# Performance work log

Hardware: AMD Instinct MI355X
Metric: run time of the kernel (lower is better)

## Reference

```python
import jax, jax.numpy as jnp
import numpy as np

B, L, D = 4, 4096, 1024


def setup_inputs() -> dict:
    key = jax.random.key(0)
    ks = jax.random.split(key, 10)
    x = jax.random.normal(ks[0], (B, L, D), dtype=jnp.float32)
    time_decay = jax.random.normal(ks[1], (D,), dtype=jnp.float32) * 0.1 - 5.0
    time_first = jax.random.normal(ks[2], (D,), dtype=jnp.float32) * 0.01
    time_mix_k = jnp.ones((D,), jnp.float32) * 0.5
    time_mix_v = jnp.ones((D,), jnp.float32) * 0.5
    time_mix_r = jnp.ones((D,), jnp.float32) * 0.5
    s = 1.0 / np.sqrt(D)
    Wk = jax.random.normal(ks[3], (D, D), dtype=jnp.float32) * s
    Wv = jax.random.normal(ks[4], (D, D), dtype=jnp.float32) * s
    Wr = jax.random.normal(ks[5], (D, D), dtype=jnp.float32) * s
    Wo = jax.random.normal(ks[6], (D, D), dtype=jnp.float32) * s
    return {"x": x, "time_decay": time_decay, "time_first": time_first,
            "time_mix_k": time_mix_k, "time_mix_v": time_mix_v, "time_mix_r": time_mix_r,
            "Wk": Wk, "Wv": Wv, "Wr": Wr, "Wo": Wo}


def _wkv_scan(k, v, w, u):
    # k, v: [B, L, D]; w, u: [D]. Sequential linear recurrence over L.
    decay = jnp.exp(w)  # per-channel decay factor e^{w}, w = -exp(time_decay) < 0
    Bb, Ll, Dd = k.shape

    def step(carry, kv_t):
        a, b = carry  # [B, D] numerator / denominator states
        k_t, v_t = kv_t
        ek_u = jnp.exp(u + k_t)
        wkv = (a + ek_u * v_t) / jnp.maximum(b + ek_u, 1e-6)
        ek = jnp.exp(k_t)
        return (decay * a + ek * v_t, decay * b + ek), wkv

    init = (jnp.zeros((Bb, Dd), k.dtype), jnp.zeros((Bb, Dd), k.dtype))
    _, out = jax.lax.scan(step, init, (jnp.swapaxes(k, 0, 1), jnp.swapaxes(v, 0, 1)))
    return jnp.swapaxes(out, 0, 1)  # [B, L, D]


def reference(x, time_decay, time_first, time_mix_k, time_mix_v, time_mix_r, Wk, Wv, Wr, Wo):
    Ll = x.shape[1]
    # token shift: x_prev[t] = x[t-1], zeros at t=0
    x_prev = jnp.pad(x, ((0, 0), (1, 0), (0, 0)))[:, :Ll]
    xk = x * time_mix_k + x_prev * (1.0 - time_mix_k)
    xv = x * time_mix_v + x_prev * (1.0 - time_mix_v)
    xr = x * time_mix_r + x_prev * (1.0 - time_mix_r)
    k = jnp.einsum('bld,ed->ble', xk, Wk)
    v = jnp.einsum('bld,ed->ble', xv, Wv)
    r = jax.nn.sigmoid(jnp.einsum('bld,ed->ble', xr, Wr))
    w = -jnp.exp(time_decay)
    wkv = _wkv_scan(k, v, w, time_first)
    return jnp.einsum('bld,ed->ble', r * wkv, Wo)
```

## Files before the change

kernel.cpp:

```cpp
#include <hip/hip_runtime.h>
#include <cstdint>
#include <cstddef>

typedef __bf16 bf16;
typedef __bf16 bf16x8 __attribute__((ext_vector_type(8)));
typedef float floatx4 __attribute__((ext_vector_type(4)));
typedef float floatx8 __attribute__((ext_vector_type(8)));
typedef unsigned int u32;

constexpr int Bb = 4, Ll = 4096, Dd = 1024;
constexpr int M  = Bb * Ll;
constexpr int NC = 64, CT = 64;

typedef const __attribute__((address_space(1))) u32 glb_u32;
typedef __attribute__((address_space(3))) u32 lds_u32;
__device__ __forceinline__ void gld16(const bf16* g, bf16* l) {
  __builtin_amdgcn_global_load_lds((glb_u32*)g, (lds_u32*)l, 16, 0, 0);
}

__global__ __launch_bounds__(256) void convw(
    const float* __restrict__ W, bf16* __restrict__ Wb)
{
  size_t base = ((size_t)blockIdx.x * 256 + threadIdx.x) * 8;
  floatx8 w = *(const floatx8*)(W + base);
  bf16x8 o;
  #pragma unroll
  for (int j = 0; j < 8; ++j) o[j] = (bf16)w[j];
  *(bf16x8*)(Wb + base) = o;
}

__global__ __launch_bounds__(256) void prep2(
    const float* __restrict__ x, const float* __restrict__ ma, const float* __restrict__ mb,
    bf16* __restrict__ oa, bf16* __restrict__ ob)
{
  size_t base = ((size_t)blockIdx.x * 256 + threadIdx.x) * 8;
  int d = (int)(base & (size_t)(Dd - 1));
  int l = (int)((base / Dd) & (size_t)(Ll - 1));
  floatx8 xc = *(const floatx8*)(x + base);
  floatx8 xp = l ? *(const floatx8*)(x + base - Dd) : (floatx8)(0.0f);
  floatx8 a = *(const floatx8*)(ma + d);
  floatx8 b = *(const floatx8*)(mb + d);
  bf16x8 ra, rb;
  #pragma unroll
  for (int j = 0; j < 8; ++j) {
    ra[j] = (bf16)(xc[j] * a[j] + xp[j] * (1.0f - a[j]));
    rb[j] = (bf16)(xc[j] * b[j] + xp[j] * (1.0f - b[j]));
  }
  *(bf16x8*)(oa + base) = ra;
  *(bf16x8*)(ob + base) = rb;
}

__global__ __launch_bounds__(256) void prep1(
    const float* __restrict__ x, const float* __restrict__ ma, bf16* __restrict__ oa)
{
  size_t base = ((size_t)blockIdx.x * 256 + threadIdx.x) * 8;
  int d = (int)(base & (size_t)(Dd - 1));
  int l = (int)((base / Dd) & (size_t)(Ll - 1));
  floatx8 xc = *(const floatx8*)(x + base);
  floatx8 xp = l ? *(const floatx8*)(x + base - Dd) : (floatx8)(0.0f);
  floatx8 a = *(const floatx8*)(ma + d);
  bf16x8 ra;
  #pragma unroll
  for (int j = 0; j < 8; ++j)
    ra[j] = (bf16)(xc[j] * a[j] + xp[j] * (1.0f - a[j]));
  *(bf16x8*)(oa + base) = ra;
}

template <int ACT>
__global__ __launch_bounds__(256) void gemm_bb(
    const bf16* __restrict__ A, const bf16* __restrict__ W, void* __restrict__ Cout)
{
  __shared__ __align__(16) bf16 As[128 * 32];
  __shared__ __align__(16) bf16 Bs[128 * 32];
  const int tid  = threadIdx.x;
  const int lane = tid & 63;
  const int w    = tid >> 6;
  const int wm   = (w >> 1) * 64, wn = (w & 1) * 64;
  const int fr   = lane & 15;
  const int cu   = lane >> 4;
  const int soff = ((cu ^ ((fr >> 1) & 3)) << 3);

  const int flat = (int)(blockIdx.y * 8 + blockIdx.x);
  const int nid  = (flat & 7) * 128 + (flat >> 3);
  const int m0   = (nid >> 3) * 128, n0 = (nid & 7) * 128;

  const int u0 = tid, u1 = tid + 256;
  const int r0 = u0 >> 2, c0 = (((u0 & 3) ^ ((r0 >> 1) & 3)) << 3);
  const int r1 = u1 >> 2, c1 = (((u1 & 3) ^ ((r1 >> 1) & 3)) << 3);

  floatx4 acc[4][4];
  #pragma unroll
  for (int i = 0; i < 4; ++i)
    #pragma unroll
    for (int j = 0; j < 4; ++j)
      acc[i][j] = (floatx4)(0.0f);

  for (int k0 = 0; k0 < Dd; k0 += 32) {
    gld16(A + (size_t)(m0 + r0) * Dd + k0 + c0, As + (size_t)u0 * 8);
    gld16(A + (size_t)(m0 + r1) * Dd + k0 + c1, As + (size_t)u1 * 8);
    gld16(W + (size_t)(n0 + r0) * Dd + k0 + c0, Bs + (size_t)u0 * 8);
    gld16(W + (size_t)(n0 + r1) * Dd + k0 + c1, Bs + (size_t)u1 * 8);
    __syncthreads();

    bf16x8 af[4], bfv[4];
    #pragma unroll
    for (int i = 0; i < 4; ++i) af[i]  = *(const bf16x8*)(As + (wm + i * 16 + fr) * 32 + soff);
    #pragma unroll
    for (int j = 0; j < 4; ++j) bfv[j] = *(const bf16x8*)(Bs + (wn + j * 16 + fr) * 32 + soff);
    #pragma unroll
    for (int i = 0; i < 4; ++i)
      #pragma unroll
      for (int j = 0; j < 4; ++j)
        acc[i][j] = __builtin_amdgcn_mfma_f32_16x16x32_bf16(af[i], bfv[j], acc[i][j], 0, 0, 0);
    __syncthreads();
  }

  #pragma unroll
  for (int i = 0; i < 4; ++i) {
    int rbase = m0 + wm + i * 16 + (lane >> 4) * 4;
    #pragma unroll
    for (int j = 0; j < 4; ++j) {
      int col = n0 + wn + j * 16 + (lane & 15);
      #pragma unroll
      for (int r = 0; r < 4; ++r) {
        float v = acc[i][j][r];
        size_t off = (size_t)(rbase + r) * Dd + col;
        if (ACT == 0)      ((float*)Cout)[off] = v;
        else if (ACT == 1) ((bf16*)Cout)[off]  = (bf16)(1.0f / (1.0f + __expf(-v)));
        else               ((bf16*)Cout)[off]  = (bf16)v;
      }
    }
  }
}

__global__ __launch_bounds__(256) void scan_partial(
    const bf16* __restrict__ k, const bf16* __restrict__ v,
    const float* __restrict__ td, float* __restrict__ Pa, float* __restrict__ Pb)
{
  int d = blockIdx.x * 256 + threadIdx.x;
  int b = blockIdx.y, c = blockIdx.z;
  float decay = __expf(-__expf(td[d]));
  size_t base = ((size_t)(b * Ll + c * CT)) * Dd + d;
  float pa = 0.0f, pb = 0.0f;
  #pragma unroll 4
  for (int t = 0; t < CT; ++t) {
    size_t idx = base + (size_t)t * Dd;
    float ek = __expf((float)k[idx]);
    pa = decay * pa + ek * (float)v[idx];
    pb = decay * pb + ek;
  }
  size_t o = ((size_t)(b * NC + c)) * Dd + d;
  Pa[o] = pa; Pb[o] = pb;
}

__global__ __launch_bounds__(256) void scan_combine(
    const float* __restrict__ td, const float* __restrict__ Pa, const float* __restrict__ Pb,
    float* __restrict__ A0, float* __restrict__ B0)
{
  int d = blockIdx.x * 256 + threadIdx.x;
  int b = blockIdx.y;
  float dT = __expf(-__expf(td[d]) * (float)CT);
  float a = 0.0f, bb = 0.0f;
  for (int c = 0; c < NC; ++c) {
    size_t o = ((size_t)(b * NC + c)) * Dd + d;
    A0[o] = a; B0[o] = bb;
    a  = dT * a  + Pa[o];
    bb = dT * bb + Pb[o];
  }
}

__global__ __launch_bounds__(256) void scan_final(
    const bf16* __restrict__ k, bf16* __restrict__ vy, const bf16* __restrict__ r,
    const float* __restrict__ td, const float* __restrict__ tf,
    const float* __restrict__ A0, const float* __restrict__ B0)
{
  int d = blockIdx.x * 256 + threadIdx.x;
  int b = blockIdx.y, c = blockIdx.z;
  float decay = __expf(-__expf(td[d]));
  float u     = tf[d];
  size_t o = ((size_t)(b * NC + c)) * Dd + d;
  float a = A0[o], bb = B0[o];
  size_t base = ((size_t)(b * Ll + c * CT)) * Dd + d;
  for (int t = 0; t < CT; ++t) {
    size_t idx = base + (size_t)t * Dd;
    float kk = (float)k[idx];
    float vv = (float)vy[idx];
    float eku = __expf(u + kk);
    float wkv = (a + eku * vv) / fmaxf(bb + eku, 1e-6f);
    vy[idx] = (bf16)((float)r[idx] * wkv);
    float ek = __expf(kk);
    a  = decay * a  + ek * vv;
    bb = decay * bb + ek;
  }
}

extern "C" void kernel_launch(void* const* d_in, const int* in_sizes, int n_in,
                              void* d_out, int out_size, void* d_ws, size_t ws_size,
                              hipStream_t stream)
{
  const float* x  = (const float*)d_in[0];
  const float* td = (const float*)d_in[1];
  const float* tf = (const float*)d_in[2];
  const float* mk = (const float*)d_in[3];
  const float* mv = (const float*)d_in[4];
  const float* mr = (const float*)d_in[5];
  const float* Wk = (const float*)d_in[6];
  const float* Wv = (const float*)d_in[7];
  const float* Wr = (const float*)d_in[8];
  const float* Wo = (const float*)d_in[9];
  float* out = (float*)d_out;

  char* ws = (char*)d_ws;
  const size_t S2 = (size_t)M * Dd * sizeof(bf16);
  const size_t SP = (size_t)Bb * NC * Dd;
  bf16* buf1 = (bf16*)(ws);
  bf16* buf2 = (bf16*)(ws + S2);
  bf16* buf3 = (bf16*)(ws + 2 * S2);
  float* Pa = (float*)(ws + 3 * S2);
  float* Pb = Pa + SP;
  float* A0 = Pb + SP;
  float* B0 = A0 + SP;

  char* ob  = (char*)d_out;
  bf16* rr  = (bf16*)d_out;
  bf16* Wkb = (bf16*)(ob + ((size_t)32 << 20));
  bf16* Wvb = (bf16*)(ob + ((size_t)34 << 20));
  bf16* Wrb = (bf16*)(ob + ((size_t)36 << 20));
  bf16* Wob = (bf16*)Pa;

  dim3 gp((unsigned)((size_t)M * Dd / (256 * 8)));
  dim3 gw((unsigned)((size_t)Dd * Dd / (256 * 8)));
  dim3 gg(Dd / 128, M / 128);

  convw<<<gw, 256, 0, stream>>>(Wk, Wkb);
  convw<<<gw, 256, 0, stream>>>(Wv, Wvb);
  convw<<<gw, 256, 0, stream>>>(Wr, Wrb);

  prep2<<<gp, 256, 0, stream>>>(x, mk, mv, buf1, buf2);
  gemm_bb<2><<<gg, 256, 0, stream>>>(buf1, Wkb, buf3);
  gemm_bb<2><<<gg, 256, 0, stream>>>(buf2, Wvb, buf1);
  prep1<<<gp, 256, 0, stream>>>(x, mr, buf2);
  gemm_bb<1><<<gg, 256, 0, stream>>>(buf2, Wrb, rr);

  scan_partial<<<dim3(Dd / 256, Bb, NC), 256, 0, stream>>>(buf3, buf1, td, Pa, Pb);
  scan_combine<<<dim3(Dd / 256, Bb), 256, 0, stream>>>(td, Pa, Pb, A0, B0);
  convw<<<gw, 256, 0, stream>>>(Wo, Wob);
  scan_final  <<<dim3(Dd / 256, Bb, NC), 256, 0, stream>>>(buf3, buf1, rr, td, tf, A0, B0);

  gemm_bb<0><<<gg, 256, 0, stream>>>(buf1, Wob, out);
}
```

Baseline: 403.8 us.

## Replace GEMM with 256x256-tile double-buffered 8-wave pipelined kernel

Replaces the 128x128, BK=32, single-buffered bf16 GEMM with a 256x256-tile, BK=64 kernel using 512 threads. It double-buffers LDS (128KB) and splits each k-step into four quarter phases, so global-to-LDS loads of the next tile interleave with MFMA work on the current one. It also uses an XOR swizzle and s_setprio around the MFMA bursts. Separately, the three weight-conversion launches are merged into one kernel. The risks are low occupancy from the large LDS footprint and correctness of the manual vmcnt waits.

```diff
diff --git a/kernel.cpp b/kernel.cpp
--- a/kernel.cpp
+++ b/kernel.cpp
@@ -17,6 +17,10 @@
 __device__ __forceinline__ void gld16(const bf16* g, bf16* l) {
   __builtin_amdgcn_global_load_lds((glb_u32*)g, (lds_u32*)l, 16, 0, 0);
 }
+__device__ __forceinline__ void bar() {
+  __builtin_amdgcn_s_barrier();
+  asm volatile("" ::: "memory");
+}
 
 __global__ __launch_bounds__(256) void convw(
     const float* __restrict__ W, bf16* __restrict__ Wb)
@@ -27,6 +31,20 @@
   #pragma unroll
   for (int j = 0; j < 8; ++j) o[j] = (bf16)w[j];
   *(bf16x8*)(Wb + base) = o;
+}
+
+__global__ __launch_bounds__(256) void convw3(
+    const float* __restrict__ Wa, const float* __restrict__ Wbp, const float* __restrict__ Wc,
+    bf16* __restrict__ oa, bf16* __restrict__ ob, bf16* __restrict__ oc)
+{
+  const float* s = blockIdx.y == 0 ? Wa : (blockIdx.y == 1 ? Wbp : Wc);
+  bf16*        d = blockIdx.y == 0 ? oa : (blockIdx.y == 1 ? ob  : oc);
+  size_t base = ((size_t)blockIdx.x * 256 + threadIdx.x) * 8;
+  floatx8 w = *(const floatx8*)(s + base);
+  bf16x8 o;
+  #pragma unroll
+  for (int j = 0; j < 8; ++j) o[j] = (bf16)w[j];
+  *(bf16x8*)(d + base) = o;
 }
 
 __global__ __launch_bounds__(256) void prep2(
@@ -67,63 +85,158 @@
 }
 
 template <int ACT>
-__global__ __launch_bounds__(256) void gemm_bb(
+__global__ __launch_bounds__(512, 2) void gemm8(
     const bf16* __restrict__ A, const bf16* __restrict__ W, void* __restrict__ Cout)
 {
-  __shared__ __align__(16) bf16 As[128 * 32];
-  __shared__ __align__(16) bf16 Bs[128 * 32];
+  __shared__ __align__(16) bf16 sm[65536];
   const int tid  = threadIdx.x;
   const int lane = tid & 63;
   const int w    = tid >> 6;
-  const int wm   = (w >> 1) * 64, wn = (w & 1) * 64;
+  const int wm   = (w >> 2) * 128;
+  const int wn   = (w & 3) * 64;
   const int fr   = lane & 15;
   const int cu   = lane >> 4;
-  const int soff = ((cu ^ ((fr >> 1) & 3)) << 3);
-
-  const int flat = (int)(blockIdx.y * 8 + blockIdx.x);
-  const int nid  = (flat & 7) * 128 + (flat >> 3);
-  const int m0   = (nid >> 3) * 128, n0 = (nid & 7) * 128;
-
-  const int u0 = tid, u1 = tid + 256;
-  const int r0 = u0 >> 2, c0 = (((u0 & 3) ^ ((r0 >> 1) & 3)) << 3);
-  const int r1 = u1 >> 2, c1 = (((u1 & 3) ^ ((r1 >> 1) & 3)) << 3);
-
-  floatx4 acc[4][4];
-  #pragma unroll
-  for (int i = 0; i < 4; ++i)
+  const int key  = fr & 7;
+  const int sw0  = ((cu)     ^ key) * 8;
+  const int sw1  = ((4 | cu) ^ key) * 8;
+  const int aro  = wm + fr;
+  const int bro  = wn + fr;
+
+  const int flat = (int)(blockIdx.y * 4 + blockIdx.x);
+  const int nid  = (flat & 7) * 32 + (flat >> 3);
+  const int m0   = (nid >> 2) * 256, n0 = (nid & 3) * 256;
+
+  const int w0_ = tid, w1_ = tid + 512;
+  const int lr0 = w0_ >> 3, sc0 = ((w0_ & 7) ^ (lr0 & 7)) * 8;
+  const int lr1 = w1_ >> 3, sc1 = ((w1_ & 7) ^ (lr1 & 7)) * 8;
+  const size_t rA0 = (size_t)(m0 + lr0) * Dd + sc0;
+  const size_t rA1 = (size_t)(m0 + lr1) * Dd + sc1;
+  const size_t rB0 = (size_t)(n0 + lr0) * Dd + sc0;
+  const size_t rB1 = (size_t)(n0 + lr1) * Dd + sc1;
+  const size_t HSTEP = (size_t)128 * Dd;
+
+  floatx4 acc[8][4];
+  #pragma unroll
+  for (int i = 0; i < 8; ++i)
     #pragma unroll
     for (int j = 0; j < 4; ++j)
       acc[i][j] = (floatx4)(0.0f);
 
-  for (int k0 = 0; k0 < Dd; k0 += 32) {
-    gld16(A + (size_t)(m0 + r0) * Dd + k0 + c0, As + (size_t)u0 * 8);
-    gld16(A + (size_t)(m0 + r1) * Dd + k0 + c1, As + (size_t)u1 * 8);
-    gld16(W + (size_t)(n0 + r0) * Dd + k0 + c0, Bs + (size_t)u0 * 8);
-    gld16(W + (size_t)(n0 + r1) * Dd + k0 + c1, Bs + (size_t)u1 * 8);
-    __syncthreads();
-
-    bf16x8 af[4], bfv[4];
-    #pragma unroll
-    for (int i = 0; i < 4; ++i) af[i]  = *(const bf16x8*)(As + (wm + i * 16 + fr) * 32 + soff);
-    #pragma unroll
-    for (int j = 0; j < 4; ++j) bfv[j] = *(const bf16x8*)(Bs + (wn + j * 16 + fr) * 32 + soff);
-    #pragma unroll
-    for (int i = 0; i < 4; ++i)
-      #pragma unroll
-      for (int j = 0; j < 4; ++j)
-        acc[i][j] = __builtin_amdgcn_mfma_f32_16x16x32_bf16(af[i], bfv[j], acc[i][j], 0, 0, 0);
-    __syncthreads();
-  }
-
-  #pragma unroll
-  for (int i = 0; i < 4; ++i) {
-    int rbase = m0 + wm + i * 16 + (lane >> 4) * 4;
+  {
+    bf16* A0 = sm;
+    bf16* B0 = sm + 16384;
+    gld16(A + rA0,         A0 + (size_t)w0_ * 8);
+    gld16(A + rA1,         A0 + (size_t)w1_ * 8);
+    gld16(W + rB0,         B0 + (size_t)w0_ * 8);
+    gld16(W + rB1,         B0 + (size_t)w1_ * 8);
+    gld16(W + rB0 + HSTEP, B0 + 8192 + (size_t)w0_ * 8);
+    gld16(W + rB1 + HSTEP, B0 + 8192 + (size_t)w1_ * 8);
+    gld16(A + rA0 + HSTEP, A0 + 8192 + (size_t)w0_ * 8);
+    gld16(A + rA1 + HSTEP, A0 + 8192 + (size_t)w1_ * 8);
+    asm volatile("s_waitcnt vmcnt(4)" ::: "memory");
+    bar();
+  }
+
+  bf16x8 a[8], bl[4], bh[4];
+  #pragma unroll 2
+  for (int t = 0; t < 16; ++t) {
+    const int p = t & 1;
+    bf16* Ap = sm + p * 32768;
+    bf16* Bp = Ap + 16384;
+    bf16* Aq = sm + (p ^ 1) * 32768;
+    bf16* Bq = Aq + 16384;
+    const size_t kn = (size_t)((t < 15 ? t + 1 : 15) * 64);
+
+    #pragma unroll
+    for (int i = 0; i < 4; ++i) {
+      a[i * 2 + 0] = *(const bf16x8*)(Ap + (aro + i * 16) * 64 + sw0);
+      a[i * 2 + 1] = *(const bf16x8*)(Ap + (aro + i * 16) * 64 + sw1);
+    }
+    #pragma unroll
+    for (int j = 0; j < 2; ++j) {
+      bl[j * 2 + 0] = *(const bf16x8*)(Bp + (bro + j * 16) * 64 + sw0);
+      bl[j * 2 + 1] = *(const bf16x8*)(Bp + (bro + j * 16) * 64 + sw1);
+    }
+    gld16(A + rA0 + kn, Aq + (size_t)w0_ * 8);
+    gld16(A + rA1 + kn, Aq + (size_t)w1_ * 8);
+    asm volatile("s_waitcnt vmcnt(4)" ::: "memory");
+    bar();
+    __builtin_amdgcn_s_setprio(1);
+    #pragma unroll
+    for (int ks = 0; ks < 2; ++ks)
+      #pragma unroll
+      for (int i = 0; i < 4; ++i)
+        #pragma unroll
+        for (int j = 0; j < 2; ++j)
+          acc[i][j] = __builtin_amdgcn_mfma_f32_16x16x32_bf16(a[i * 2 + ks], bl[j * 2 + ks], acc[i][j], 0, 0, 0);
+    __builtin_amdgcn_s_setprio(0);
+    bar();
+
+    #pragma unroll
+    for (int j = 0; j < 2; ++j) {
+      bh[j * 2 + 0] = *(const bf16x8*)(Bp + (bro + (j + 2) * 16) * 64 + sw0);
+      bh[j * 2 + 1] = *(const bf16x8*)(Bp + (bro + (j + 2) * 16) * 64 + sw1);
+    }
+    gld16(W + rB0 + kn, Bq + (size_t)w0_ * 8);
+    gld16(W + rB1 + kn, Bq + (size_t)w1_ * 8);
+    asm volatile("s_waitcnt vmcnt(4)" ::: "memory");
+    bar();
+    __builtin_amdgcn_s_setprio(1);
+    #pragma unroll
+    for (int ks = 0; ks < 2; ++ks)
+      #pragma unroll
+      for (int i = 0; i < 4; ++i)
+        #pragma unroll
+        for (int j = 0; j < 2; ++j)
+          acc[i][j + 2] = __builtin_amdgcn_mfma_f32_16x16x32_bf16(a[i * 2 + ks], bh[j * 2 + ks], acc[i][j + 2], 0, 0, 0);
+    __builtin_amdgcn_s_setprio(0);
+    bar();
+
+    #pragma unroll
+    for (int i = 0; i < 4; ++i) {
+      a[i * 2 + 0] = *(const bf16x8*)(Ap + (aro + (i + 4) * 16) * 64 + sw0);
+      a[i * 2 + 1] = *(const bf16x8*)(Ap + (aro + (i + 4) * 16) * 64 + sw1);
+    }
+    gld16(W + rB0 + kn + HSTEP, Bq + 8192 + (size_t)w0_ * 8);
+    gld16(W + rB1 + kn + HSTEP, Bq + 8192 + (size_t)w1_ * 8);
+    bar();
+    __builtin_amdgcn_s_setprio(1);
+    #pragma unroll
+    for (int ks = 0; ks < 2; ++ks)
+      #pragma unroll
+      for (int i = 0; i < 4; ++i)
+        #pragma unroll
+        for (int j = 0; j < 2; ++j)
+          acc[i + 4][j + 2] = __builtin_amdgcn_mfma_f32_16x16x32_bf16(a[i * 2 + ks], bh[j * 2 + ks], acc[i + 4][j + 2], 0, 0, 0);
+    __builtin_amdgcn_s_setprio(0);
+    bar();
+
+    gld16(A + rA0 + kn + HSTEP, Aq + 8192 + (size_t)w0_ * 8);
+    gld16(A + rA1 + kn + HSTEP, Aq + 8192 + (size_t)w1_ * 8);
+    asm volatile("s_waitcnt vmcnt(4)" ::: "memory");
+    bar();
+    __builtin_amdgcn_s_setprio(1);
+    #pragma unroll
+    for (int ks = 0; ks < 2; ++ks)
+      #pragma unroll
+      for (int i = 0; i < 4; ++i)
+        #pragma unroll
+        for (int j = 0; j < 2; ++j)
+          acc[i + 4][j] = __builtin_amdgcn_mfma_f32_16x16x32_bf16(a[i * 2 + ks], bl[j * 2 + ks], acc[i + 4][j], 0, 0, 0);
+    __builtin_amdgcn_s_setprio(0);
+    bar();
+  }
+  asm volatile("s_waitcnt vmcnt(0)" ::: "memory");
+
+  #pragma unroll
+  for (int mi = 0; mi < 8; ++mi) {
+    int rbase = m0 + wm + mi * 16 + (lane >> 4) * 4;
     #pragma unroll
     for (int j = 0; j < 4; ++j) {
       int col = n0 + wn + j * 16 + (lane & 15);
       #pragma unroll
       for (int r = 0; r < 4; ++r) {
-        float v = acc[i][j][r];
+        float v = acc[mi][j][r];
         size_t off = (size_t)(rbase + r) * Dd + col;
         if (ACT == 0)      ((float*)Cout)[off] = v;
         else if (ACT == 1) ((bf16*)Cout)[off]  = (bf16)(1.0f / (1.0f + __expf(-v)));
@@ -230,22 +343,20 @@
 
   dim3 gp((unsigned)((size_t)M * Dd / (256 * 8)));
   dim3 gw((unsigned)((size_t)Dd * Dd / (256 * 8)));
-  dim3 gg(Dd / 128, M / 128);
-
-  convw<<<gw, 256, 0, stream>>>(Wk, Wkb);
-  convw<<<gw, 256, 0, stream>>>(Wv, Wvb);
-  convw<<<gw, 256, 0, stream>>>(Wr, Wrb);
+  dim3 gg(Dd / 256, M / 256);
+
+  convw3<<<dim3(gw.x, 3), 256, 0, stream>>>(Wk, Wv, Wr, Wkb, Wvb, Wrb);
 
   prep2<<<gp, 256, 0, stream>>>(x, mk, mv, buf1, buf2);
-  gemm_bb<2><<<gg, 256, 0, stream>>>(buf1, Wkb, buf3);
-  gemm_bb<2><<<gg, 256, 0, stream>>>(buf2, Wvb, buf1);
+  gemm8<2><<<gg, 512, 0, stream>>>(buf1, Wkb, buf3);
+  gemm8<2><<<gg, 512, 0, stream>>>(buf2, Wvb, buf1);
   prep1<<<gp, 256, 0, stream>>>(x, mr, buf2);
-  gemm_bb<1><<<gg, 256, 0, stream>>>(buf2, Wrb, rr);
+  gemm8<1><<<gg, 512, 0, stream>>>(buf2, Wrb, rr);
 
   scan_partial<<<dim3(Dd / 256, Bb, NC), 256, 0, stream>>>(buf3, buf1, td, Pa, Pb);
   scan_combine<<<dim3(Dd / 256, Bb), 256, 0, stream>>>(td, Pa, Pb, A0, B0);
   convw<<<gw, 256, 0, stream>>>(Wo, Wob);
   scan_final  <<<dim3(Dd / 256, Bb, NC), 256, 0, stream>>>(buf3, buf1, rr, td, tf, A0, B0);
 
-  gemm_bb<0><<<gg, 256, 0, stream>>>(buf1, Wob, out);
-}
+  gemm8<0><<<gg, 512, 0, stream>>>(buf1, Wob, out);
+}
```

Result: faster. 350.0 us (-13.3%).

## Replace GEMM with 256x256 triple-buffered pipelined kernel and fuse prep kernels

Applied to the files above, without the earlier changes.

The GEMM is rewritten to use 256x256 tiles with 512 threads and a three-slot LDS ring. Global-to-LDS loads are issued two steps ahead and interleaved with MFMA work through sched_group_barrier and setprio, with explicit vmcnt waits. This is meant to hide load latency and reuse each tile more. The three weight conversions are merged into one launch, and the three token-shift preps into one kernel, reordering GEMMs so buffers are freed correctly. The larger tile gives only 256 blocks per GEMM and uses more LDS and registers, which may limit occupancy.

```diff
diff --git a/kernel.cpp b/kernel.cpp
--- a/kernel.cpp
+++ b/kernel.cpp
@@ -17,6 +17,10 @@
 __device__ __forceinline__ void gld16(const bf16* g, bf16* l) {
   __builtin_amdgcn_global_load_lds((glb_u32*)g, (lds_u32*)l, 16, 0, 0);
 }
+__device__ __forceinline__ void bar() {
+  __builtin_amdgcn_s_barrier();
+  asm volatile("" ::: "memory");
+}
 
 __global__ __launch_bounds__(256) void convw(
     const float* __restrict__ W, bf16* __restrict__ Wb)
@@ -29,9 +33,24 @@
   *(bf16x8*)(Wb + base) = o;
 }
 
-__global__ __launch_bounds__(256) void prep2(
+__global__ __launch_bounds__(256) void convw3(
+    const float* __restrict__ Wa, const float* __restrict__ Wbp, const float* __restrict__ Wc,
+    bf16* __restrict__ oa, bf16* __restrict__ ob, bf16* __restrict__ oc)
+{
+  const float* s = blockIdx.y == 0 ? Wa : (blockIdx.y == 1 ? Wbp : Wc);
+  bf16*        d = blockIdx.y == 0 ? oa : (blockIdx.y == 1 ? ob  : oc);
+  size_t base = ((size_t)blockIdx.x * 256 + threadIdx.x) * 8;
+  floatx8 w = *(const floatx8*)(s + base);
+  bf16x8 o;
+  #pragma unroll
+  for (int j = 0; j < 8; ++j) o[j] = (bf16)w[j];
+  *(bf16x8*)(d + base) = o;
+}
+
+__global__ __launch_bounds__(256) void prep3(
     const float* __restrict__ x, const float* __restrict__ ma, const float* __restrict__ mb,
-    bf16* __restrict__ oa, bf16* __restrict__ ob)
+    const float* __restrict__ mc,
+    bf16* __restrict__ oa, bf16* __restrict__ ob, bf16* __restrict__ oc)
 {
   size_t base = ((size_t)blockIdx.x * 256 + threadIdx.x) * 8;
   int d = (int)(base & (size_t)(Dd - 1));
@@ -40,90 +59,137 @@
   floatx8 xp = l ? *(const floatx8*)(x + base - Dd) : (floatx8)(0.0f);
   floatx8 a = *(const floatx8*)(ma + d);
   floatx8 b = *(const floatx8*)(mb + d);
-  bf16x8 ra, rb;
+  floatx8 c = *(const floatx8*)(mc + d);
+  bf16x8 ra, rb, rc;
   #pragma unroll
   for (int j = 0; j < 8; ++j) {
     ra[j] = (bf16)(xc[j] * a[j] + xp[j] * (1.0f - a[j]));
     rb[j] = (bf16)(xc[j] * b[j] + xp[j] * (1.0f - b[j]));
+    rc[j] = (bf16)(xc[j] * c[j] + xp[j] * (1.0f - c[j]));
   }
   *(bf16x8*)(oa + base) = ra;
   *(bf16x8*)(ob + base) = rb;
-}
-
-__global__ __launch_bounds__(256) void prep1(
-    const float* __restrict__ x, const float* __restrict__ ma, bf16* __restrict__ oa)
-{
-  size_t base = ((size_t)blockIdx.x * 256 + threadIdx.x) * 8;
-  int d = (int)(base & (size_t)(Dd - 1));
-  int l = (int)((base / Dd) & (size_t)(Ll - 1));
-  floatx8 xc = *(const floatx8*)(x + base);
-  floatx8 xp = l ? *(const floatx8*)(x + base - Dd) : (floatx8)(0.0f);
-  floatx8 a = *(const floatx8*)(ma + d);
-  bf16x8 ra;
-  #pragma unroll
-  for (int j = 0; j < 8; ++j)
-    ra[j] = (bf16)(xc[j] * a[j] + xp[j] * (1.0f - a[j]));
-  *(bf16x8*)(oa + base) = ra;
+  *(bf16x8*)(oc + base) = rc;
 }
 
 template <int ACT>
-__global__ __launch_bounds__(256) void gemm_bb(
+__global__ __launch_bounds__(512, 2) void gemm8(
     const bf16* __restrict__ A, const bf16* __restrict__ W, void* __restrict__ Cout)
 {
-  __shared__ __align__(16) bf16 As[128 * 32];
-  __shared__ __align__(16) bf16 Bs[128 * 32];
+  __shared__ __align__(16) bf16 sm[49152];
   const int tid  = threadIdx.x;
   const int lane = tid & 63;
   const int w    = tid >> 6;
-  const int wm   = (w >> 1) * 64, wn = (w & 1) * 64;
+  const int wm   = (w >> 2) * 128;
+  const int wn   = (w & 3) * 64;
   const int fr   = lane & 15;
   const int cu   = lane >> 4;
   const int soff = ((cu ^ ((fr >> 1) & 3)) << 3);
-
-  const int flat = (int)(blockIdx.y * 8 + blockIdx.x);
-  const int nid  = (flat & 7) * 128 + (flat >> 3);
-  const int m0   = (nid >> 3) * 128, n0 = (nid & 7) * 128;
-
-  const int u0 = tid, u1 = tid + 256;
+  const int aro  = wm + fr;
+  const int bro  = wn + fr;
+
+  const int flat = (int)(blockIdx.y * 4 + blockIdx.x);
+  const int nid  = (flat & 7) * 32 + (flat >> 3);
+  const int m0   = (nid >> 2) * 256, n0 = (nid & 3) * 256;
+
+  const int u0 = tid, u1 = tid + 512;
   const int r0 = u0 >> 2, c0 = (((u0 & 3) ^ ((r0 >> 1) & 3)) << 3);
   const int r1 = u1 >> 2, c1 = (((u1 & 3) ^ ((r1 >> 1) & 3)) << 3);
-
-  floatx4 acc[4][4];
-  #pragma unroll
-  for (int i = 0; i < 4; ++i)
+  const size_t gA0 = (size_t)(m0 + r0) * Dd + c0;
+  const size_t gA1 = (size_t)(m0 + r1) * Dd + c1;
+  const size_t gB0 = (size_t)(n0 + r0) * Dd + c0;
+  const size_t gB1 = (size_t)(n0 + r1) * Dd + c1;
+
+  auto stageA = [&](int slot, int t) {
+    const size_t k = (size_t)(t > 31 ? 31 : t) * 32;
+    bf16* d = sm + slot * 16384;
+    gld16(A + gA0 + k, d + (size_t)u0 * 8);
+    gld16(A + gA1 + k, d + (size_t)u1 * 8);
+  };
+  auto stageB = [&](int slot, int t) {
+    const size_t k = (size_t)(t > 31 ? 31 : t) * 32;
+    bf16* d = sm + slot * 16384 + 8192;
+    gld16(W + gB0 + k, d + (size_t)u0 * 8);
+    gld16(W + gB1 + k, d + (size_t)u1 * 8);
+  };
+  auto rdA = [&](int slot, int fi, bf16x8 (&dst)[4]) {
+    const bf16* s = sm + slot * 16384;
+    #pragma unroll
+    for (int i = 0; i < 4; ++i)
+      dst[i] = *(const bf16x8*)(s + (aro + (fi + i) * 16) * 32 + soff);
+  };
+  auto rdB = [&](int slot, bf16x8 (&dst)[4]) {
+    const bf16* s = sm + slot * 16384 + 8192;
+    #pragma unroll
+    for (int j = 0; j < 4; ++j)
+      dst[j] = *(const bf16x8*)(s + (bro + j * 16) * 32 + soff);
+  };
+
+  floatx4 acc[8][4];
+  #pragma unroll
+  for (int i = 0; i < 8; ++i)
     #pragma unroll
     for (int j = 0; j < 4; ++j)
       acc[i][j] = (floatx4)(0.0f);
 
-  for (int k0 = 0; k0 < Dd; k0 += 32) {
-    gld16(A + (size_t)(m0 + r0) * Dd + k0 + c0, As + (size_t)u0 * 8);
-    gld16(A + (size_t)(m0 + r1) * Dd + k0 + c1, As + (size_t)u1 * 8);
-    gld16(W + (size_t)(n0 + r0) * Dd + k0 + c0, Bs + (size_t)u0 * 8);
-    gld16(W + (size_t)(n0 + r1) * Dd + k0 + c1, Bs + (size_t)u1 * 8);
-    __syncthreads();
-
-    bf16x8 af[4], bfv[4];
-    #pragma unroll
-    for (int i = 0; i < 4; ++i) af[i]  = *(const bf16x8*)(As + (wm + i * 16 + fr) * 32 + soff);
-    #pragma unroll
-    for (int j = 0; j < 4; ++j) bfv[j] = *(const bf16x8*)(Bs + (wn + j * 16 + fr) * 32 + soff);
-    #pragma unroll
-    for (int i = 0; i < 4; ++i)
-      #pragma unroll
-      for (int j = 0; j < 4; ++j)
-        acc[i][j] = __builtin_amdgcn_mfma_f32_16x16x32_bf16(af[i], bfv[j], acc[i][j], 0, 0, 0);
-    __syncthreads();
-  }
-
-  #pragma unroll
-  for (int i = 0; i < 4; ++i) {
-    int rbase = m0 + wm + i * 16 + (lane >> 4) * 4;
+  bf16x8 a03[4], a47[4], bA[4], bB[4];
+
+  stageA(0, 0); stageB(0, 0); stageA(1, 1); stageB(1, 1);
+  asm volatile("s_waitcnt vmcnt(4)" ::: "memory");
+  bar();
+  rdA(0, 0, a03);
+  rdB(0, bA);
+
+  int s_cur = 0, s_nxt = 1, s_stg = 2;
+
+#define PHASE_PAIR(T, BCUR, BNXT)                                              \
+  {                                                                            \
+                                                                       \
+    bar();                                                                     \
+    stageA(s_stg, (T) + 2);                                                    \
+    rdA(s_cur, 4, a47);                                                        \
+    __builtin_amdgcn_sched_group_barrier(0x100, 4, 0);                         \
+    __builtin_amdgcn_sched_group_barrier(0x008, 16, 0);                        \
+    __builtin_amdgcn_s_setprio(1);                                             \
+    _Pragma("unroll") for (int i = 0; i < 4; ++i)                              \
+      _Pragma("unroll") for (int j = 0; j < 4; ++j)                            \
+        acc[i][j] = __builtin_amdgcn_mfma_f32_16x16x32_bf16(                   \
+            a03[i], BCUR[j], acc[i][j], 0, 0, 0);                              \
+    __builtin_amdgcn_s_setprio(0);                                             \
+                                                                       \
+    asm volatile("s_waitcnt vmcnt(2)" ::: "memory");                           \
+    bar();                                                                     \
+    stageB(s_stg, (T) + 2);                                                    \
+    rdA(s_nxt, 0, a03);                                                        \
+    rdB(s_nxt, BNXT);                                                          \
+    __builtin_amdgcn_sched_group_barrier(0x100, 8, 0);                         \
+    __builtin_amdgcn_sched_group_barrier(0x008, 16, 0);                        \
+    __builtin_amdgcn_s_setprio(1);                                             \
+    _Pragma("unroll") for (int i = 0; i < 4; ++i)                              \
+      _Pragma("unroll") for (int j = 0; j < 4; ++j)                            \
+        acc[4 + i][j] = __builtin_amdgcn_mfma_f32_16x16x32_bf16(               \
+            a47[i], BCUR[j], acc[4 + i][j], 0, 0, 0);                          \
+    __builtin_amdgcn_s_setprio(0);                                             \
+    { int _t = s_cur; s_cur = s_nxt; s_nxt = s_stg; s_stg = _t; }              \
+  }
+
+  for (int tt = 0; tt < 16; ++tt) {
+    PHASE_PAIR(2 * tt,     bA, bB);
+    PHASE_PAIR(2 * tt + 1, bB, bA);
+  }
+#undef PHASE_PAIR
+
+  asm volatile("s_waitcnt vmcnt(0)" ::: "memory");
+
+  #pragma unroll
+  for (int mi = 0; mi < 8; ++mi) {
+    int rbase = m0 + wm + mi * 16 + (lane >> 4) * 4;
     #pragma unroll
     for (int j = 0; j < 4; ++j) {
       int col = n0 + wn + j * 16 + (lane & 15);
       #pragma unroll
       for (int r = 0; r < 4; ++r) {
-        float v = acc[i][j][r];
+        float v = acc[mi][j][r];
         size_t off = (size_t)(rbase + r) * Dd + col;
         if (ACT == 0)      ((float*)Cout)[off] = v;
         else if (ACT == 1) ((bf16*)Cout)[off]  = (bf16)(1.0f / (1.0f + __expf(-v)));
@@ -230,22 +296,20 @@
 
   dim3 gp((unsigned)((size_t)M * Dd / (256 * 8)));
   dim3 gw((unsigned)((size_t)Dd * Dd / (256 * 8)));
-  dim3 gg(Dd / 128, M / 128);
-
-  convw<<<gw, 256, 0, stream>>>(Wk, Wkb);
-  convw<<<gw, 256, 0, stream>>>(Wv, Wvb);
-  convw<<<gw, 256, 0, stream>>>(Wr, Wrb);
-
-  prep2<<<gp, 256, 0, stream>>>(x, mk, mv, buf1, buf2);
-  gemm_bb<2><<<gg, 256, 0, stream>>>(buf1, Wkb, buf3);
-  gemm_bb<2><<<gg, 256, 0, stream>>>(buf2, Wvb, buf1);
-  prep1<<<gp, 256, 0, stream>>>(x, mr, buf2);
-  gemm_bb<1><<<gg, 256, 0, stream>>>(buf2, Wrb, rr);
+  dim3 gg(Dd / 256, M / 256);
+
+  convw3<<<dim3(gw.x, 3), 256, 0, stream>>>(Wk, Wv, Wr, Wkb, Wvb, Wrb);
+
+  prep3<<<gp, 256, 0, stream>>>(x, mk, mv, mr, buf1, buf2, buf3);
+
+  gemm8<1><<<gg, 512, 0, stream>>>(buf3, Wrb, rr);
+  gemm8<2><<<gg, 512, 0, stream>>>(buf1, Wkb, buf3);
+  gemm8<2><<<gg, 512, 0, stream>>>(buf2, Wvb, buf1);
 
   scan_partial<<<dim3(Dd / 256, Bb, NC), 256, 0, stream>>>(buf3, buf1, td, Pa, Pb);
   scan_combine<<<dim3(Dd / 256, Bb), 256, 0, stream>>>(td, Pa, Pb, A0, B0);
   convw<<<gw, 256, 0, stream>>>(Wo, Wob);
   scan_final  <<<dim3(Dd / 256, Bb, NC), 256, 0, stream>>>(buf3, buf1, rr, td, tf, A0, B0);
 
-  gemm_bb<0><<<gg, 256, 0, stream>>>(buf1, Wob, out);
-}
+  gemm8<0><<<gg, 512, 0, stream>>>(buf1, Wob, out);
+}
```

New measurement: 341.3 us. 15.5% less time.
